# Kernel optimization log

Measured on AMD Instinct MI355X. Metric: run time of the kernel, lower is better.

The kernel has to match this reference:

```python
import jax, jax.numpy as jnp
import numpy as np

B, S, D, H = 4, 2048, 1024, 16
HD = D // H


def setup_inputs() -> dict:
    key = jax.random.key(0)
    ks = jax.random.split(key, 12)
    scale = 1.0 / np.sqrt(D)
    q = jax.random.normal(ks[0], (B, S, D), jnp.float32)
    k = jax.random.normal(ks[1], (B, S, D), jnp.float32)
    v = jax.random.normal(ks[2], (B, S, D), jnp.float32)
    mask = jax.random.randint(ks[3], (B, S, S), 0, 2).astype(bool)
    Wq = jax.random.normal(ks[4], (D, D), jnp.float32) * scale
    bq = jnp.zeros((D,), jnp.float32)
    Wk = jax.random.normal(ks[5], (D, D), jnp.float32) * scale
    bk = jnp.zeros((D,), jnp.float32)
    Wv = jax.random.normal(ks[6], (D, D), jnp.float32) * scale
    bv = jnp.zeros((D,), jnp.float32)
    Wo = jax.random.normal(ks[7], (D, D), jnp.float32) * scale
    bo = jnp.zeros((D,), jnp.float32)
    return {"q": q, "k": k, "v": v, "mask": mask,
            "Wq": Wq, "bq": bq, "Wk": Wk, "bk": bk,
            "Wv": Wv, "bv": bv, "Wo": Wo, "bo": bo}


def reference(q, k, v, mask, Wq, bq, Wk, bk, Wv, bv, Wo, bo):
    # project and split heads: [B,S,D] -> [B,H,S,HD]
    def split_heads(x, W, b):
        y = x @ W + b
        return y.reshape(B, S, H, HD).transpose(0, 2, 1, 3)

    Q = split_heads(q, Wq, bq)
    K = split_heads(k, Wk, bk)
    V = split_heads(v, Wv, bv)
    inv_sqrt_dk = 1.0 / np.sqrt(HD)
    scores = jnp.einsum('bhqd,bhkd->bhqk', Q, K) * inv_sqrt_dk
    scores = jnp.where(mask[:, None, :, :], -1e9, scores)
    attn = jax.nn.softmax(scores, axis=-1)
    ctx = jnp.einsum('bhqk,bhkd->bhqd', attn, V)  # [B,H,S,HD]
    ctx = ctx.transpose(0, 2, 1, 3).reshape(B, S, D)
    return ctx @ Wo + bo
```

## Files before the change

kernel.cpp:

```cpp
#include <hip/hip_runtime.h>
#include <stdint.h>

#define B_ 4
#define S_ 2048
#define D_ 1024
#define H_ 16
#define HD_ 64

typedef __attribute__((ext_vector_type(8))) __bf16          bf16x8;
typedef __attribute__((ext_vector_type(8))) unsigned short  u16x8;
typedef __attribute__((ext_vector_type(4))) unsigned short  u16x4;
typedef __attribute__((ext_vector_type(4))) float           f32x4;
typedef __attribute__((ext_vector_type(16))) float          f32x16;
typedef unsigned short u16;
typedef unsigned int   u32;
typedef unsigned long long u64;

union BF8 { u16x8 u; bf16x8 b; u32 w[4]; };

__device__ __forceinline__ u16 f2bf(float f) {
  union { float f; uint32_t u; } v; v.f = f;
  uint32_t r = (v.u + 0x7FFFu + ((v.u >> 16) & 1u)) >> 16;
  return (u16)r;
}

__device__ __forceinline__ u32 cvtpk(float lo, float hi) {
  u32 r;
  asm("v_cvt_pk_bf16_f32 %0, %1, %2" : "=v"(r) : "v"(lo), "v"(hi));
  return r;
}

__device__ __forceinline__ float fexp2(float x) {
  float r;
  asm("v_exp_f32 %0, %1" : "=v"(r) : "v"(x));
  return r;
}

__device__ __forceinline__ float frcp(float x) {
  float r;
  asm("v_rcp_f32 %0, %1" : "=v"(r) : "v"(x));
  return r;
}

__device__ __forceinline__ void pswap(u32& a, u32& b) {
  asm("v_permlane32_swap_b32 %0, %1" : "+v"(a), "+v"(b));
}

__device__ __forceinline__ float andf(float x, u32 m) {
  union { float f; u32 u; } v; v.f = x; v.u &= m; return v.f;
}

typedef const unsigned int __attribute__((address_space(1)))* gas1_t;
typedef unsigned int __attribute__((address_space(3)))*       las3_t;

__device__ __forceinline__ void gll16(const void* g, void* l) {
  __builtin_amdgcn_global_load_lds((gas1_t)g, (las3_t)l, 16, 0, 0);
}

#define MFMA32(a, b, c) __builtin_amdgcn_mfma_f32_32x32x16_bf16((a), (b), (c), 0, 0, 0)

__global__ __launch_bounds__(256) void prep_k(const float* __restrict__ qi, const float* __restrict__ ki,
                                              const float* __restrict__ vi, u16* __restrict__ oq,
                                              u16* __restrict__ ok, u16* __restrict__ ov,
                                              const float* __restrict__ Wq, const float* __restrict__ Wk,
                                              const float* __restrict__ Wv, const float* __restrict__ Wo,
                                              u16* __restrict__ Tq, u16* __restrict__ Tk,
                                              u16* __restrict__ Tv, u16* __restrict__ To) {
  __shared__ float tile[64][65];
  int blk = blockIdx.x;
  int t = threadIdx.x;
  if (blk < 12288) {
    const float* in; u16* out;
    if (blk < 4096) { in = qi; out = oq; }
    else if (blk < 8192) { in = ki; out = ok; blk -= 4096; }
    else { in = vi; out = ov; blk -= 8192; }
    int i = blk * 256 + t;
    const float4* p = ((const float4*)in) + (size_t)i * 2;
    float4 a = p[0], b = p[1];
    u16x8 o;
    o[0] = f2bf(a.x); o[1] = f2bf(a.y); o[2] = f2bf(a.z); o[3] = f2bf(a.w);
    o[4] = f2bf(b.x); o[5] = f2bf(b.y); o[6] = f2bf(b.z); o[7] = f2bf(b.w);
    *(((u16x8*)out) + i) = o;
    return;
  }
  int wi = blk - 12288;
  int z = wi >> 8, rem = wi & 255;
  int bx = rem & 15, by = rem >> 4;
  const float* src; u16* dst;
  switch (z) {
    case 0: src = Wq; dst = Tq; break;
    case 1: src = Wk; dst = Tk; break;
    case 2: src = Wv; dst = Tv; break;
    default: src = Wo; dst = To; break;
  }
  int k0 = bx * 64, n0 = by * 64;
#pragma unroll
  for (int it = 0; it < 4; ++it) {
    int idx = it * 256 + t;
    int r = idx >> 4, c = idx & 15;
    float4 v = *(const float4*)(src + (size_t)(k0 + r) * 1024 + n0 + c * 4);
    tile[r][c * 4 + 0] = v.x; tile[r][c * 4 + 1] = v.y;
    tile[r][c * 4 + 2] = v.z; tile[r][c * 4 + 3] = v.w;
  }
  __syncthreads();
#pragma unroll
  for (int it = 0; it < 2; ++it) {
    int idx = it * 256 + t;
    int n = idx >> 3, kc = idx & 7;
    u16x8 o;
#pragma unroll
    for (int j = 0; j < 8; ++j) o[j] = f2bf(tile[kc * 8 + j][n]);
    *(u16x8*)(dst + (size_t)(n0 + n) * 1024 + k0 + kc * 8) = o;
  }
}

__global__ __launch_bounds__(256) void maskpack_k(const void* __restrict__ mraw,
                                                  u64* __restrict__ mout) {
  const u32* hdr = (const u32*)mraw;
  int t = threadIdx.x;
  int lane = t & 63;
  u32 hv = hdr[lane];
  bool isf = (hv == 0x3F800000u);
  u64 bigm = __ballot(hv > 1u && !isf);
  u64 fm = __ballot(isf);
  int fmt = (__popcll(fm) > 8) ? 2 : ((bigm != 0ull) ? 0 : 1);
  size_t idx = (size_t)blockIdx.x * 256 + t;
  u64 bits = 0;
  if (fmt == 0) {
    const u64* p = (const u64*)((const uint8_t*)mraw + idx * 64);
#pragma unroll
    for (int j = 0; j < 8; ++j) {
      u64 v = p[j];
#pragma unroll
      for (int kk = 0; kk < 8; ++kk)
        bits |= (u64)(((v >> (8 * kk)) & 0xFFull) != 0) << (j * 8 + kk);
    }
  } else if (fmt == 1) {
    const int* p = ((const int*)mraw) + idx * 64;
#pragma unroll
    for (int j = 0; j < 64; ++j) bits |= (u64)(p[j] != 0) << j;
  } else {
    const u32* p = ((const u32*)mraw) + idx * 64;
#pragma unroll
    for (int j = 0; j < 64; ++j) bits |= (u64)((p[j] << 1) != 0) << j;
  }
  mout[idx] = bits;
}

__global__ __launch_bounds__(256) void proj3_k(const u16* __restrict__ Aq, const u16* __restrict__ Ak,
                                               const u16* __restrict__ Av,
                                               const u16* __restrict__ Tq, const u16* __restrict__ Tk,
                                               const u16* __restrict__ Tv,
                                               const float* __restrict__ bq, const float* __restrict__ bk,
                                               const float* __restrict__ bv,
                                               u16* __restrict__ Qh, u16* __restrict__ Kh,
                                               u16* __restrict__ Vt, float qscale) {
  int g = blockIdx.x >> 9, bid = blockIdx.x & 511;
  const u16* A; const u16* Bt; const float* bias; u16* outp; float scale;
  if (g == 0) { A = Aq; Bt = Tq; bias = bq; outp = Qh; scale = qscale; }
  else if (g == 1) { A = Ak; Bt = Tk; bias = bk; outp = Kh; scale = 1.0f; }
  else { A = Av; Bt = Tv; bias = bv; outp = Vt; scale = 1.0f; }
  int xcd = bid & 7, loc = bid >> 3;
  int mt = xcd * 8 + (loc & 7), nt = loc >> 3;
  int m0 = mt * 128, n0 = nt * 128;
  int t = threadIdx.x, w = t >> 6, lane = t & 63;
  int l15 = lane & 15, l4 = lane >> 4;
  int wm = w >> 1, wn = w & 1;
  __shared__ __align__(16) char smem[16384];
  const f32x4 vzero = {0.f, 0.f, 0.f, 0.f};
  f32x4 acc[4][4];
#pragma unroll
  for (int a = 0; a < 4; ++a)
#pragma unroll
    for (int c = 0; c < 4; ++c) acc[a][c] = vzero;

  for (int k0 = 0; k0 < 1024; k0 += 32) {
#pragma unroll
    for (int i = 0; i < 2; ++i) {
      int chunk = i * 256 + w * 64 + lane;
      int row = chunk >> 2, slot = chunk & 3;
      int sc = slot ^ ((row >> 1) & 3);
      gll16(A + (size_t)(m0 + row) * 1024 + k0 + sc * 8, smem + (i * 256 + w * 64) * 16);
      gll16(Bt + (size_t)(n0 + row) * 1024 + k0 + sc * 8, smem + 8192 + (i * 256 + w * 64) * 16);
    }
    __syncthreads();
    BF8 am[4], bn[4];
#pragma unroll
    for (int mb = 0; mb < 4; ++mb) {
      int row = wm * 64 + mb * 16 + l15;
      int sl = l4 ^ ((row >> 1) & 3);
      am[mb].u = *(const u16x8*)(smem + row * 64 + sl * 16);
    }
#pragma unroll
    for (int nb = 0; nb < 4; ++nb) {
      int row = wn * 64 + nb * 16 + l15;
      int sl = l4 ^ ((row >> 1) & 3);
      bn[nb].u = *(const u16x8*)(smem + 8192 + row * 64 + sl * 16);
    }
#pragma unroll
    for (int mb = 0; mb < 4; ++mb)
#pragma unroll
      for (int nb = 0; nb < 4; ++nb)
        acc[mb][nb] = __builtin_amdgcn_mfma_f32_16x16x32_bf16(am[mb].b, bn[nb].b, acc[mb][nb], 0, 0, 0);
    __syncthreads();
  }
  if (g == 2) {
#pragma unroll
    for (int mb = 0; mb < 4; ++mb)
#pragma unroll
      for (int nb = 0; nb < 4; ++nb) {
        int no = n0 + wn * 64 + nb * 16 + l15;
        int h = no >> 6, hd = no & 63;
        int m = m0 + wm * 64 + mb * 16 + l4 * 4;
        int bb = m >> 11, s = m & 2047;
        float bsv = bias[no];
        u16x4 ov;
#pragma unroll
        for (int r = 0; r < 4; ++r) ov[r] = f2bf(acc[mb][nb][r] + bsv);
        *(u16x4*)(outp + (((size_t)bb * H_ + h) * HD_ + hd) * S_ + s) = ov;
      }
  } else {
#pragma unroll
    for (int mb = 0; mb < 4; ++mb)
#pragma unroll
      for (int nb = 0; nb < 4; ++nb)
#pragma unroll
        for (int r = 0; r < 4; ++r) {
          int grow = m0 + wm * 64 + mb * 16 + l4 * 4 + r;
          int gcol = n0 + wn * 64 + nb * 16 + l15;
          float v = (acc[mb][nb][r] + bias[gcol]) * scale;
          int bb = grow >> 11, s = grow & 2047, h = gcol >> 6, hd = gcol & 63;
          outp[(((size_t)bb * H_ + h) * S_ + s) * HD_ + hd] = f2bf(v);
        }
  }
}

__global__ __launch_bounds__(256) void gemmo_k(const u16* __restrict__ A,
                                               const u16* __restrict__ Bt,
                                               const float* __restrict__ bias,
                                               float* __restrict__ outp) {
  int bid = blockIdx.x;
  int xcd = bid & 7, loc = bid >> 3;
  int mt = xcd * 8 + (loc & 7), nt = loc >> 3;
  int m0 = mt * 128, n0 = nt * 128;
  int t = threadIdx.x, w = t >> 6, lane = t & 63;
  int l15 = lane & 15, l4 = lane >> 4;
  int wm = w >> 1, wn = w & 1;
  __shared__ __align__(16) char smem[16384];
  const f32x4 vzero = {0.f, 0.f, 0.f, 0.f};
  f32x4 acc[4][4];
#pragma unroll
  for (int a = 0; a < 4; ++a)
#pragma unroll
    for (int c = 0; c < 4; ++c) acc[a][c] = vzero;

  for (int k0 = 0; k0 < 1024; k0 += 32) {
#pragma unroll
    for (int i = 0; i < 2; ++i) {
      int chunk = i * 256 + w * 64 + lane;
      int row = chunk >> 2, slot = chunk & 3;
      int sc = slot ^ ((row >> 1) & 3);
      gll16(A + (size_t)(m0 + row) * 1024 + k0 + sc * 8, smem + (i * 256 + w * 64) * 16);
      gll16(Bt + (size_t)(n0 + row) * 1024 + k0 + sc * 8, smem + 8192 + (i * 256 + w * 64) * 16);
    }
    __syncthreads();
    BF8 am[4], bn[4];
#pragma unroll
    for (int mb = 0; mb < 4; ++mb) {
      int row = wm * 64 + mb * 16 + l15;
      int sl = l4 ^ ((row >> 1) & 3);
      am[mb].u = *(const u16x8*)(smem + row * 64 + sl * 16);
    }
#pragma unroll
    for (int nb = 0; nb < 4; ++nb) {
      int row = wn * 64 + nb * 16 + l15;
      int sl = l4 ^ ((row >> 1) & 3);
      bn[nb].u = *(const u16x8*)(smem + 8192 + row * 64 + sl * 16);
    }
#pragma unroll
    for (int mb = 0; mb < 4; ++mb)
#pragma unroll
      for (int nb = 0; nb < 4; ++nb)
        acc[mb][nb] = __builtin_amdgcn_mfma_f32_16x16x32_bf16(am[mb].b, bn[nb].b, acc[mb][nb], 0, 0, 0);
    __syncthreads();
  }
#pragma unroll
  for (int mb = 0; mb < 4; ++mb)
#pragma unroll
    for (int nb = 0; nb < 4; ++nb)
#pragma unroll
      for (int r = 0; r < 4; ++r) {
        int grow = m0 + wm * 64 + mb * 16 + l4 * 4 + r;
        int gcol = n0 + wn * 64 + nb * 16 + l15;
        outp[(size_t)grow * 1024 + gcol] = acc[mb][nb][r] + bias[gcol];
      }
}

__global__ __launch_bounds__(256) void flash_k(const u16* __restrict__ Qh,
                                               const u16* __restrict__ Kh,
                                               const u16* __restrict__ Vt,
                                               const u64* __restrict__ mb,
                                               u16* __restrict__ ctx) {
  int bid = blockIdx.x;
  int xcd = bid & 7, loc = bid >> 3;
  int bh = xcd * 8 + (loc & 7);
  int qblk = loc >> 3;
  int b = bh >> 4, h = bh & 15;
  int t = threadIdx.x, w = t >> 6, lane = t & 63;
  int l31 = lane & 31, l5 = lane >> 5;
  __shared__ __align__(16) char smem[32768];

  int q0 = qblk * 128 + w * 32;
  const u16* kbase = Kh + (size_t)bh * S_ * HD_;
  const u16* vbase = Vt + (size_t)bh * HD_ * S_;
  const uint2* mrow = ((const uint2*)mb) + ((size_t)b * S_ + q0 + l31) * 32;

  const u16* qbase = Qh + ((size_t)bh * S_ + q0 + l31) * HD_;
  BF8 qf[4];
#pragma unroll
  for (int dk = 0; dk < 4; ++dk) qf[dk].u = *(const u16x8*)(qbase + dk * 16 + l5 * 8);

  int koff0[4], koffB[4];
#pragma unroll
  for (int dk = 0; dk < 4; ++dk) {
    int s0_ = (dk * 2 + l5) ^ (l31 & 7) ^ (l31 >> 3);
    koff0[dk] = l31 * 128 + s0_ * 16;
    koffB[dk] = 4096 + l31 * 128 + ((s0_ ^ 4) * 16);
  }

  BF8 onesf;
#pragma unroll
  for (int i = 0; i < 8; ++i) onesf.u[i] = 0x3F80;

  f32x16 o0, o1, lac, zv;
#pragma unroll
  for (int r = 0; r < 16; ++r) { o0[r] = 0.f; o1[r] = 0.f; lac[r] = 0.f; zv[r] = 0.f; }

#define STAGE(KT, BUF)                                                          \
  do {                                                                          \
    char* Kd = smem + (BUF);                                                    \
    int k0s = (KT) * 64;                                                        \
    _Pragma("unroll") for (int i_ = 0; i_ < 2; ++i_) {                          \
      int c_ = i_ * 256 + t;                                                    \
      int row_ = c_ >> 3, sl_ = c_ & 7;                                         \
      int sc_ = sl_ ^ (row_ & 7) ^ (row_ >> 3);                                 \
      int cw_ = (i_ * 256 + w * 64) * 16;                                       \
      gll16(kbase + (size_t)(k0s + row_) * HD_ + sc_ * 8, Kd + cw_);            \
      gll16(vbase + (size_t)row_ * S_ + k0s + sc_ * 8, Kd + 8192 + cw_);        \
    }                                                                           \
  } while (0)

#define MKFRAG(FR, A0, B0, C0, D0)                                              \
  do {                                                                          \
    u32 xx0 = (A0), xx1 = (C0), yy0 = (B0), yy1 = (D0);                         \
    pswap(xx0, xx1); pswap(yy0, yy1);                                           \
    FR.w[0] = xx0; FR.w[1] = yy0; FR.w[2] = xx1; FR.w[3] = yy1;                 \
  } while (0)

#define PVS(FR, KC)                                                             \
  do {                                                                          \
    lac = MFMA32(FR.b, onesf.b, lac);                                           \
    BF8 vf0, vf1;                                                               \
    vf0.u = *(const u16x8*)(Kb + 8192 + koff0[(KC)]);                           \
    vf1.u = *(const u16x8*)(Kb + 8192 + koffB[(KC)]);                           \
    o0 = MFMA32(FR.b, vf0.b, o0);                                               \
    o1 = MFMA32(FR.b, vf1.b, o1);                                               \
  } while (0)

#define FTILE(KT, BUF, OBUF, ISLAST)                                            \
  {                                                                             \
    __syncthreads();                                                            \
    uint2 mw = mrow[(KT)];                                                      \
    if (!(ISLAST)) STAGE((KT) + 1, OBUF);                                       \
    const char* Kb = smem + (BUF);                                              \
    f32x16 sa0, sa1;                                                            \
    __builtin_amdgcn_s_setprio(1);                                              \
    {                                                                           \
      BF8 kf0, kf1;                                                             \
      kf0.u = *(const u16x8*)(Kb + koff0[0]);                                   \
      kf1.u = *(const u16x8*)(Kb + koffB[0]);                                   \
      sa0 = MFMA32(kf0.b, qf[0].b, zv);                                         \
      sa1 = MFMA32(kf1.b, qf[0].b, zv);                                         \
    }                                                                           \
    _Pragma("unroll") for (int dk = 1; dk < 4; ++dk) {                          \
      BF8 kf0, kf1;                                                             \
      kf0.u = *(const u16x8*)(Kb + koff0[dk]);                                  \
      kf1.u = *(const u16x8*)(Kb + koffB[dk]);                                  \
      sa0 = MFMA32(kf0.b, qf[dk].b, sa0);                                       \
      sa1 = MFMA32(kf1.b, qf[dk].b, sa1);                                       \
    }                                                                           \
    __builtin_amdgcn_s_setprio(0);                                              \
    u32 nw0 = ~(mw.x >> (l5 * 4));                                              \
    u32 nw1 = ~(mw.y >> (l5 * 4));                                              \
    _Pragma("unroll") for (int r = 0; r < 16; ++r) {                            \
      const int pp = (r & 3) + 8 * (r >> 2);                                    \
      sa0[r] = andf(fexp2(sa0[r]), (u32)__builtin_amdgcn_sbfe((int)nw0, pp, 1));\
      sa1[r] = andf(fexp2(sa1[r]), (u32)__builtin_amdgcn_sbfe((int)nw1, pp, 1));\
    }                                                                           \
    u32 pk0[8], pk1[8];                                                         \
    _Pragma("unroll") for (int i = 0; i < 8; ++i) {                             \
      pk0[i] = cvtpk(sa0[2 * i], sa0[2 * i + 1]);                               \
      pk1[i] = cvtpk(sa1[2 * i], sa1[2 * i + 1]);                               \
    }                                                                           \
    BF8 fr0, fr1, fr2, fr3;                                                     \
    MKFRAG(fr0, pk0[0], pk0[1], pk0[2], pk0[3]);                                \
    MKFRAG(fr1, pk0[4], pk0[5], pk0[6], pk0[7]);                                \
    MKFRAG(fr2, pk1[0], pk1[1], pk1[2], pk1[3]);                                \
    MKFRAG(fr3, pk1[4], pk1[5], pk1[6], pk1[7]);                                \
    __builtin_amdgcn_s_setprio(1);                                              \
    PVS(fr0, 0); PVS(fr1, 1); PVS(fr2, 2); PVS(fr3, 3);                         \
    __builtin_amdgcn_s_setprio(0);                                              \
  }

  STAGE(0, 0);
  for (int kt2 = 0; kt2 < 16; ++kt2) {
    FTILE(2 * kt2, 0, 16384, false);
    FTILE(2 * kt2 + 1, 16384, 0, (kt2 == 15));
  }

#pragma unroll
  for (int r = 0; r < 16; ++r) {
    float inv = frcp(lac[r] + 1e-35f);
    int q = (r & 3) + 8 * (r >> 2) + 4 * l5;
    size_t base = ((size_t)b * S_ + q0 + q) * D_ + h * HD_;
    ctx[base + l31]      = f2bf(o0[r] * inv);
    ctx[base + 32 + l31] = f2bf(o1[r] * inv);
  }
#undef STAGE
#undef MKFRAG
#undef PVS
#undef FTILE
}

extern "C" void kernel_launch(void* const* d_in, const int* in_sizes, int n_in,
                              void* d_out, int out_size, void* d_ws, size_t ws_size,
                              hipStream_t stream) {
  (void)in_sizes; (void)n_in; (void)out_size; (void)ws_size;
  const float* q  = (const float*)d_in[0];
  const float* k  = (const float*)d_in[1];
  const float* v  = (const float*)d_in[2];
  const void*  mk = d_in[3];
  const float* Wq = (const float*)d_in[4];
  const float* bq = (const float*)d_in[5];
  const float* Wk = (const float*)d_in[6];
  const float* bk = (const float*)d_in[7];
  const float* Wv = (const float*)d_in[8];
  const float* bv = (const float*)d_in[9];
  const float* Wo = (const float*)d_in[10];
  const float* bo = (const float*)d_in[11];

  char* ws = (char*)d_ws;
  u16* qb   = (u16*)(ws + 0);
  u16* kbuf = (u16*)(ws + 16777216);
  u16* vbuf = (u16*)(ws + 33554432);
  u16* Tq   = (u16*)(ws + 50331648);
  u16* Tk   = (u16*)(ws + 52428800);
  u16* Tv   = (u16*)(ws + 54525952);
  u16* To   = (u16*)(ws + 56623104);
  u16* Qh   = (u16*)(ws + 58720256);
  u16* Kh   = (u16*)(ws + 75497472);
  u16* Vt   = (u16*)(ws + 92274688);
  u16* ctx  = kbuf;
  u64* mc   = (u64*)vbuf;

  const float QSCALE = 0.18033688011112042f;

  prep_k<<<13312, 256, 0, stream>>>(q, k, v, qb, kbuf, vbuf,
                                    Wq, Wk, Wv, Wo, Tq, Tk, Tv, To);
  proj3_k<<<1536, 256, 0, stream>>>(qb, kbuf, vbuf, Tq, Tk, Tv,
                                    bq, bk, bv, Qh, Kh, Vt, QSCALE);
  maskpack_k<<<1024, 256, 0, stream>>>(mk, mc);
  flash_k<<<1024, 256, 0, stream>>>(Qh, Kh, Vt, mc, ctx);
  gemmo_k<<<512, 256, 0, stream>>>(ctx, To, bo, (float*)d_out);
}
```

Baseline: 250.4 us.

## Replace projection GEMMs with 256x256-tile, 4-stage pipelined 32x32 MFMA kernel

Both the QKV projection and the output projection now use a shared GEMM body with 256x256 block tiles, 512 threads, 32x32x16 MFMA instructions and a four-deep global-to-LDS prefetch ring synchronised with explicit waitcnt and barriers. This raises arithmetic intensity per block and overlaps loads with compute, replacing the single-buffered 128x128 tiles that waited on a full barrier every k-step. The cost is 128KB of LDS per block, which allows only one block per CU. Grids also shrink to 384 and 128 blocks, which may underfill a 256-CU device, especially for the output GEMM.

```diff
diff --git a/kernel.cpp b/kernel.cpp
--- a/kernel.cpp
+++ b/kernel.cpp
@@ -147,153 +147,161 @@
   mout[idx] = bits;
 }
 
-__global__ __launch_bounds__(256) void proj3_k(const u16* __restrict__ Aq, const u16* __restrict__ Ak,
-                                               const u16* __restrict__ Av,
-                                               const u16* __restrict__ Tq, const u16* __restrict__ Tk,
-                                               const u16* __restrict__ Tv,
-                                               const float* __restrict__ bq, const float* __restrict__ bk,
-                                               const float* __restrict__ bv,
-                                               u16* __restrict__ Qh, u16* __restrict__ Kh,
-                                               u16* __restrict__ Vt, float qscale) {
-  int g = blockIdx.x >> 9, bid = blockIdx.x & 511;
-  const u16* A; const u16* Bt; const float* bias; u16* outp; float scale;
-  if (g == 0) { A = Aq; Bt = Tq; bias = bq; outp = Qh; scale = qscale; }
-  else if (g == 1) { A = Ak; Bt = Tk; bias = bk; outp = Kh; scale = 1.0f; }
-  else { A = Av; Bt = Tv; bias = bv; outp = Vt; scale = 1.0f; }
-  int xcd = bid & 7, loc = bid >> 3;
-  int mt = xcd * 8 + (loc & 7), nt = loc >> 3;
-  int m0 = mt * 128, n0 = nt * 128;
-  int t = threadIdx.x, w = t >> 6, lane = t & 63;
-  int l15 = lane & 15, l4 = lane >> 4;
-  int wm = w >> 1, wn = w & 1;
-  __shared__ __align__(16) char smem[16384];
-  const f32x4 vzero = {0.f, 0.f, 0.f, 0.f};
-  f32x4 acc[4][4];
-#pragma unroll
-  for (int a = 0; a < 4; ++a)
-#pragma unroll
-    for (int c = 0; c < 4; ++c) acc[a][c] = vzero;
-
-  for (int k0 = 0; k0 < 1024; k0 += 32) {
-#pragma unroll
-    for (int i = 0; i < 2; ++i) {
-      int chunk = i * 256 + w * 64 + lane;
-      int row = chunk >> 2, slot = chunk & 3;
-      int sc = slot ^ ((row >> 1) & 3);
-      gll16(A + (size_t)(m0 + row) * 1024 + k0 + sc * 8, smem + (i * 256 + w * 64) * 16);
-      gll16(Bt + (size_t)(n0 + row) * 1024 + k0 + sc * 8, smem + 8192 + (i * 256 + w * 64) * 16);
+__device__ __forceinline__ void gemm256_body(const u16* __restrict__ A, const u16* __restrict__ Bt,
+                                             const float* __restrict__ bias, void* __restrict__ outp,
+                                             float scale, int mode, int inner, char* smem) {
+  int xcd = inner & 7, loc = inner >> 3;
+  int mt = xcd * 4 + (loc & 3), nt = loc >> 2;
+  int m0 = mt * 256, n0 = nt * 256;
+  int tid = threadIdx.x, w = tid >> 6, lane = tid & 63;
+  int l31 = lane & 31, l5 = lane >> 5;
+  int wm = w >> 2, wn = w & 3;
+
+  const u16* pA[2]; const u16* pB[2];
+#pragma unroll
+  for (int q = 0; q < 2; ++q) {
+    int c = q * 512 + tid;
+    int R = c >> 3, s8 = c & 7;
+    int s8u = s8 ^ (R & 7) ^ ((R >> 3) & 7);
+    int srow = 2 * R + (s8u >> 2), skw = s8u & 3;
+    pA[q] = A  + ((size_t)(m0 + srow) << 10) + skw * 8;
+    pB[q] = Bt + ((size_t)(n0 + srow) << 10) + skw * 8;
+  }
+
+  int aoff[4][2], boff[2][2];
+#pragma unroll
+  for (int i = 0; i < 4; ++i) {
+    int r = wm * 128 + i * 32 + l31;
+    int R = r >> 1, sw = (R & 7) ^ ((R >> 3) & 7);
+#pragma unroll
+    for (int kk = 0; kk < 2; ++kk) {
+      int s8 = ((r & 1) << 2) + kk * 2 + l5;
+      aoff[i][kk] = R * 128 + ((s8 ^ sw) << 4);
     }
-    __syncthreads();
-    BF8 am[4], bn[4];
-#pragma unroll
-    for (int mb = 0; mb < 4; ++mb) {
-      int row = wm * 64 + mb * 16 + l15;
-      int sl = l4 ^ ((row >> 1) & 3);
-      am[mb].u = *(const u16x8*)(smem + row * 64 + sl * 16);
+  }
+#pragma unroll
+  for (int j = 0; j < 2; ++j) {
+    int r = wn * 64 + j * 32 + l31;
+    int R = r >> 1, sw = (R & 7) ^ ((R >> 3) & 7);
+#pragma unroll
+    for (int kk = 0; kk < 2; ++kk) {
+      int s8 = ((r & 1) << 2) + kk * 2 + l5;
+      boff[j][kk] = 32768 + R * 128 + ((s8 ^ sw) << 4);
     }
-#pragma unroll
-    for (int nb = 0; nb < 4; ++nb) {
-      int row = wn * 64 + nb * 16 + l15;
-      int sl = l4 ^ ((row >> 1) & 3);
-      bn[nb].u = *(const u16x8*)(smem + 8192 + row * 64 + sl * 16);
+  }
+
+  f32x16 acc[4][2];
+#pragma unroll
+  for (int i = 0; i < 4; ++i)
+#pragma unroll
+    for (int j = 0; j < 2; ++j)
+#pragma unroll
+      for (int r = 0; r < 16; ++r) acc[i][j][r] = 0.f;
+
+#define GSTAGE(TAU)                                                             \
+  do {                                                                          \
+    char* db = smem + ((((TAU) >> 1) & 1) << 16) + (((TAU) & 1) << 14) + w * 1024; \
+    gll16(pA[0] + (TAU) * 32, db);                                              \
+    gll16(pA[1] + (TAU) * 32, db + 8192);                                       \
+    gll16(pB[0] + (TAU) * 32, db + 32768);                                      \
+    gll16(pB[1] + (TAU) * 32, db + 40960);                                      \
+  } while (0)
+
+#define GCOMPUTE(TAU)                                                           \
+  do {                                                                          \
+    const char* base = smem + ((((TAU) >> 1) & 1) << 16) + (((TAU) & 1) << 14); \
+    BF8 af[4][2], bf_[2][2];                                                    \
+    _Pragma("unroll") for (int kk = 0; kk < 2; ++kk) {                          \
+      _Pragma("unroll") for (int i = 0; i < 4; ++i)                             \
+        af[i][kk].u = *(const u16x8*)(base + aoff[i][kk]);                      \
+      _Pragma("unroll") for (int j = 0; j < 2; ++j)                             \
+        bf_[j][kk].u = *(const u16x8*)(base + boff[j][kk]);                     \
+    }                                                                           \
+    __builtin_amdgcn_s_setprio(1);                                              \
+    _Pragma("unroll") for (int kk = 0; kk < 2; ++kk)                            \
+      _Pragma("unroll") for (int i = 0; i < 4; ++i)                             \
+        _Pragma("unroll") for (int j = 0; j < 2; ++j)                           \
+          acc[i][j] = MFMA32(af[i][kk].b, bf_[j][kk].b, acc[i][j]);             \
+    __builtin_amdgcn_s_setprio(0);                                              \
+  } while (0)
+
+  GSTAGE(0);
+  GSTAGE(1);
+#pragma unroll 2
+  for (int tau = 0; tau < 31; ++tau) {
+    asm volatile("s_waitcnt vmcnt(4)" ::: "memory");
+    __builtin_amdgcn_s_barrier();
+    __builtin_amdgcn_sched_barrier(0);
+    if (tau < 30) GSTAGE(tau + 2);
+    GCOMPUTE(tau);
+  }
+  asm volatile("s_waitcnt vmcnt(0)" ::: "memory");
+  __builtin_amdgcn_s_barrier();
+  __builtin_amdgcn_sched_barrier(0);
+  GCOMPUTE(31);
+#undef GSTAGE
+#undef GCOMPUTE
+
+#pragma unroll
+  for (int i = 0; i < 4; ++i)
+#pragma unroll
+    for (int j = 0; j < 2; ++j) {
+      int gcol = n0 + wn * 64 + j * 32 + l31;
+      float bv = bias[gcol];
+      if (mode == 1) {
+        int hh = gcol >> 6, hd = gcol & 63;
+#pragma unroll
+        for (int qd = 0; qd < 4; ++qd) {
+          int grow = m0 + wm * 128 + i * 32 + qd * 8 + l5 * 4;
+          int bb = grow >> 11, s = grow & 2047;
+          u16x4 ov;
+#pragma unroll
+          for (int rr = 0; rr < 4; ++rr) ov[rr] = f2bf(acc[i][j][qd * 4 + rr] + bv);
+          *(u16x4*)((u16*)outp + (((size_t)bb * H_ + hh) * HD_ + hd) * S_ + s) = ov;
+        }
+      } else if (mode == 0) {
+        int hh = gcol >> 6, hd = gcol & 63;
+#pragma unroll
+        for (int reg = 0; reg < 16; ++reg) {
+          int grow = m0 + wm * 128 + i * 32 + (reg & 3) + 8 * (reg >> 2) + 4 * l5;
+          int bb = grow >> 11, s = grow & 2047;
+          ((u16*)outp)[(((size_t)bb * H_ + hh) * S_ + s) * HD_ + hd] =
+              f2bf((acc[i][j][reg] + bv) * scale);
+        }
+      } else {
+#pragma unroll
+        for (int reg = 0; reg < 16; ++reg) {
+          int grow = m0 + wm * 128 + i * 32 + (reg & 3) + 8 * (reg >> 2) + 4 * l5;
+          ((float*)outp)[(size_t)grow * 1024 + gcol] = acc[i][j][reg] + bv;
+        }
+      }
     }
-#pragma unroll
-    for (int mb = 0; mb < 4; ++mb)
-#pragma unroll
-      for (int nb = 0; nb < 4; ++nb)
-        acc[mb][nb] = __builtin_amdgcn_mfma_f32_16x16x32_bf16(am[mb].b, bn[nb].b, acc[mb][nb], 0, 0, 0);
-    __syncthreads();
-  }
-  if (g == 2) {
-#pragma unroll
-    for (int mb = 0; mb < 4; ++mb)
-#pragma unroll
-      for (int nb = 0; nb < 4; ++nb) {
-        int no = n0 + wn * 64 + nb * 16 + l15;
-        int h = no >> 6, hd = no & 63;
-        int m = m0 + wm * 64 + mb * 16 + l4 * 4;
-        int bb = m >> 11, s = m & 2047;
-        float bsv = bias[no];
-        u16x4 ov;
-#pragma unroll
-        for (int r = 0; r < 4; ++r) ov[r] = f2bf(acc[mb][nb][r] + bsv);
-        *(u16x4*)(outp + (((size_t)bb * H_ + h) * HD_ + hd) * S_ + s) = ov;
-      }
-  } else {
-#pragma unroll
-    for (int mb = 0; mb < 4; ++mb)
-#pragma unroll
-      for (int nb = 0; nb < 4; ++nb)
-#pragma unroll
-        for (int r = 0; r < 4; ++r) {
-          int grow = m0 + wm * 64 + mb * 16 + l4 * 4 + r;
-          int gcol = n0 + wn * 64 + nb * 16 + l15;
-          float v = (acc[mb][nb][r] + bias[gcol]) * scale;
-          int bb = grow >> 11, s = grow & 2047, h = gcol >> 6, hd = gcol & 63;
-          outp[(((size_t)bb * H_ + h) * S_ + s) * HD_ + hd] = f2bf(v);
-        }
-  }
-}
-
-__global__ __launch_bounds__(256) void gemmo_k(const u16* __restrict__ A,
-                                               const u16* __restrict__ Bt,
-                                               const float* __restrict__ bias,
-                                               float* __restrict__ outp) {
+}
+
+__global__ __launch_bounds__(512) void proj3n_k(const u16* __restrict__ Aq, const u16* __restrict__ Ak,
+                                                const u16* __restrict__ Av,
+                                                const u16* __restrict__ Tq, const u16* __restrict__ Tk,
+                                                const u16* __restrict__ Tv,
+                                                const float* __restrict__ bq, const float* __restrict__ bk,
+                                                const float* __restrict__ bv,
+                                                u16* __restrict__ Qh, u16* __restrict__ Kh,
+                                                u16* __restrict__ Vt, float qscale) {
+  __shared__ __align__(16) char smem[131072];
   int bid = blockIdx.x;
-  int xcd = bid & 7, loc = bid >> 3;
-  int mt = xcd * 8 + (loc & 7), nt = loc >> 3;
-  int m0 = mt * 128, n0 = nt * 128;
-  int t = threadIdx.x, w = t >> 6, lane = t & 63;
-  int l15 = lane & 15, l4 = lane >> 4;
-  int wm = w >> 1, wn = w & 1;
-  __shared__ __align__(16) char smem[16384];
-  const f32x4 vzero = {0.f, 0.f, 0.f, 0.f};
-  f32x4 acc[4][4];
-#pragma unroll
-  for (int a = 0; a < 4; ++a)
-#pragma unroll
-    for (int c = 0; c < 4; ++c) acc[a][c] = vzero;
-
-  for (int k0 = 0; k0 < 1024; k0 += 32) {
-#pragma unroll
-    for (int i = 0; i < 2; ++i) {
-      int chunk = i * 256 + w * 64 + lane;
-      int row = chunk >> 2, slot = chunk & 3;
-      int sc = slot ^ ((row >> 1) & 3);
-      gll16(A + (size_t)(m0 + row) * 1024 + k0 + sc * 8, smem + (i * 256 + w * 64) * 16);
-      gll16(Bt + (size_t)(n0 + row) * 1024 + k0 + sc * 8, smem + 8192 + (i * 256 + w * 64) * 16);
-    }
-    __syncthreads();
-    BF8 am[4], bn[4];
-#pragma unroll
-    for (int mb = 0; mb < 4; ++mb) {
-      int row = wm * 64 + mb * 16 + l15;
-      int sl = l4 ^ ((row >> 1) & 3);
-      am[mb].u = *(const u16x8*)(smem + row * 64 + sl * 16);
-    }
-#pragma unroll
-    for (int nb = 0; nb < 4; ++nb) {
-      int row = wn * 64 + nb * 16 + l15;
-      int sl = l4 ^ ((row >> 1) & 3);
-      bn[nb].u = *(const u16x8*)(smem + 8192 + row * 64 + sl * 16);
-    }
-#pragma unroll
-    for (int mb = 0; mb < 4; ++mb)
-#pragma unroll
-      for (int nb = 0; nb < 4; ++nb)
-        acc[mb][nb] = __builtin_amdgcn_mfma_f32_16x16x32_bf16(am[mb].b, bn[nb].b, acc[mb][nb], 0, 0, 0);
-    __syncthreads();
-  }
-#pragma unroll
-  for (int mb = 0; mb < 4; ++mb)
-#pragma unroll
-    for (int nb = 0; nb < 4; ++nb)
-#pragma unroll
-      for (int r = 0; r < 4; ++r) {
-        int grow = m0 + wm * 64 + mb * 16 + l4 * 4 + r;
-        int gcol = n0 + wn * 64 + nb * 16 + l15;
-        outp[(size_t)grow * 1024 + gcol] = acc[mb][nb][r] + bias[gcol];
-      }
+  int g = bid >> 7, inner = bid & 127;
+  const u16* A; const u16* Bt; const float* bias; void* outp; float scale; int mode;
+  if (g == 0)      { A = Aq; Bt = Tq; bias = bq; outp = Qh; scale = qscale; mode = 0; }
+  else if (g == 1) { A = Ak; Bt = Tk; bias = bk; outp = Kh; scale = 1.0f;  mode = 0; }
+  else             { A = Av; Bt = Tv; bias = bv; outp = Vt; scale = 1.0f;  mode = 1; }
+  gemm256_body(A, Bt, bias, outp, scale, mode, inner, smem);
+}
+
+__global__ __launch_bounds__(512) void gemmo2_k(const u16* __restrict__ A,
+                                                const u16* __restrict__ Bt,
+                                                const float* __restrict__ bias,
+                                                float* __restrict__ outp) {
+  __shared__ __align__(16) char smem[131072];
+  gemm256_body(A, Bt, bias, outp, 1.0f, 2, blockIdx.x, smem);
 }
 
 __global__ __launch_bounds__(256) void flash_k(const u16* __restrict__ Qh,
@@ -467,9 +475,9 @@
 
   prep_k<<<13312, 256, 0, stream>>>(q, k, v, qb, kbuf, vbuf,
                                     Wq, Wk, Wv, Wo, Tq, Tk, Tv, To);
-  proj3_k<<<1536, 256, 0, stream>>>(qb, kbuf, vbuf, Tq, Tk, Tv,
+  proj3n_k<<<384, 512, 0, stream>>>(qb, kbuf, vbuf, Tq, Tk, Tv,
                                     bq, bk, bv, Qh, Kh, Vt, QSCALE);
   maskpack_k<<<1024, 256, 0, stream>>>(mk, mc);
   flash_k<<<1024, 256, 0, stream>>>(Qh, Kh, Vt, mc, ctx);
-  gemmo_k<<<512, 256, 0, stream>>>(ctx, To, bo, (float*)d_out);
-}
+  gemmo2_k<<<128, 512, 0, stream>>>(ctx, To, bo, (float*)d_out);
+}
```

Result: slower. 268.5 us (+7.2%).

## Fuse fp32-to-bf16 activation conversion into projection GEMM A-tile loads

Applied to the files above, without the earlier changes.

The separate pass that converted q/k/v from fp32 to bf16 in workspace is removed. The projection GEMM now loads fp32 A tiles directly into registers, packs them to bf16 and writes them into swizzled LDS. This avoids writing and rereading about 48 MB of intermediate bf16 activations. In exchange, the GEMM reads twice the A bytes per tile, and those loads go through registers synchronously with no prefetch, which may expose latency in the k-loop.

```diff
diff --git a/kernel.cpp b/kernel.cpp
--- a/kernel.cpp
+++ b/kernel.cpp
@@ -59,31 +59,13 @@
 
 #define MFMA32(a, b, c) __builtin_amdgcn_mfma_f32_32x32x16_bf16((a), (b), (c), 0, 0, 0)
 
-__global__ __launch_bounds__(256) void prep_k(const float* __restrict__ qi, const float* __restrict__ ki,
-                                              const float* __restrict__ vi, u16* __restrict__ oq,
-                                              u16* __restrict__ ok, u16* __restrict__ ov,
-                                              const float* __restrict__ Wq, const float* __restrict__ Wk,
-                                              const float* __restrict__ Wv, const float* __restrict__ Wo,
-                                              u16* __restrict__ Tq, u16* __restrict__ Tk,
-                                              u16* __restrict__ Tv, u16* __restrict__ To) {
+__global__ __launch_bounds__(256) void wt_k(const float* __restrict__ Wq, const float* __restrict__ Wk,
+                                            const float* __restrict__ Wv, const float* __restrict__ Wo,
+                                            u16* __restrict__ Tq, u16* __restrict__ Tk,
+                                            u16* __restrict__ Tv, u16* __restrict__ To) {
   __shared__ float tile[64][65];
-  int blk = blockIdx.x;
   int t = threadIdx.x;
-  if (blk < 12288) {
-    const float* in; u16* out;
-    if (blk < 4096) { in = qi; out = oq; }
-    else if (blk < 8192) { in = ki; out = ok; blk -= 4096; }
-    else { in = vi; out = ov; blk -= 8192; }
-    int i = blk * 256 + t;
-    const float4* p = ((const float4*)in) + (size_t)i * 2;
-    float4 a = p[0], b = p[1];
-    u16x8 o;
-    o[0] = f2bf(a.x); o[1] = f2bf(a.y); o[2] = f2bf(a.z); o[3] = f2bf(a.w);
-    o[4] = f2bf(b.x); o[5] = f2bf(b.y); o[6] = f2bf(b.z); o[7] = f2bf(b.w);
-    *(((u16x8*)out) + i) = o;
-    return;
-  }
-  int wi = blk - 12288;
+  int wi = blockIdx.x;
   int z = wi >> 8, rem = wi & 255;
   int bx = rem & 15, by = rem >> 4;
   const float* src; u16* dst;
@@ -147,8 +129,8 @@
   mout[idx] = bits;
 }
 
-__global__ __launch_bounds__(256) void proj3_k(const u16* __restrict__ Aq, const u16* __restrict__ Ak,
-                                               const u16* __restrict__ Av,
+__global__ __launch_bounds__(256) void proj3_k(const float* __restrict__ Aq, const float* __restrict__ Ak,
+                                               const float* __restrict__ Av,
                                                const u16* __restrict__ Tq, const u16* __restrict__ Tk,
                                                const u16* __restrict__ Tv,
                                                const float* __restrict__ bq, const float* __restrict__ bk,
@@ -156,7 +138,7 @@
                                                u16* __restrict__ Qh, u16* __restrict__ Kh,
                                                u16* __restrict__ Vt, float qscale) {
   int g = blockIdx.x >> 9, bid = blockIdx.x & 511;
-  const u16* A; const u16* Bt; const float* bias; u16* outp; float scale;
+  const float* A; const u16* Bt; const float* bias; u16* outp; float scale;
   if (g == 0) { A = Aq; Bt = Tq; bias = bq; outp = Qh; scale = qscale; }
   else if (g == 1) { A = Ak; Bt = Tk; bias = bk; outp = Kh; scale = 1.0f; }
   else { A = Av; Bt = Tv; bias = bv; outp = Vt; scale = 1.0f; }
@@ -174,15 +156,29 @@
 #pragma unroll
     for (int c = 0; c < 4; ++c) acc[a][c] = vzero;
 
+  int arow = t >> 1, ahalf = t & 1;
+  const float* abase = A + (size_t)(m0 + arow) * 1024 + ahalf * 16;
+  int aswz = (arow >> 1) & 3;
+  char* adst0 = smem + arow * 64 + (((2 * ahalf) ^ aswz) << 4);
+  char* adst1 = smem + arow * 64 + (((2 * ahalf + 1) ^ aswz) << 4);
+
   for (int k0 = 0; k0 < 1024; k0 += 32) {
+    const float4* ap = (const float4*)(abase + k0);
+    float4 a0 = ap[0], a1 = ap[1], a2 = ap[2], a3 = ap[3];
 #pragma unroll
     for (int i = 0; i < 2; ++i) {
       int chunk = i * 256 + w * 64 + lane;
       int row = chunk >> 2, slot = chunk & 3;
       int sc = slot ^ ((row >> 1) & 3);
-      gll16(A + (size_t)(m0 + row) * 1024 + k0 + sc * 8, smem + (i * 256 + w * 64) * 16);
       gll16(Bt + (size_t)(n0 + row) * 1024 + k0 + sc * 8, smem + 8192 + (i * 256 + w * 64) * 16);
     }
+    uint4 wv0, wv1;
+    wv0.x = cvtpk(a0.x, a0.y); wv0.y = cvtpk(a0.z, a0.w);
+    wv0.z = cvtpk(a1.x, a1.y); wv0.w = cvtpk(a1.z, a1.w);
+    wv1.x = cvtpk(a2.x, a2.y); wv1.y = cvtpk(a2.z, a2.w);
+    wv1.z = cvtpk(a3.x, a3.y); wv1.w = cvtpk(a3.z, a3.w);
+    *(uint4*)adst0 = wv0;
+    *(uint4*)adst1 = wv1;
     __syncthreads();
     BF8 am[4], bn[4];
 #pragma unroll
@@ -450,9 +446,8 @@
   const float* bo = (const float*)d_in[11];
 
   char* ws = (char*)d_ws;
-  u16* qb   = (u16*)(ws + 0);
-  u16* kbuf = (u16*)(ws + 16777216);
-  u16* vbuf = (u16*)(ws + 33554432);
+  u16* ctx  = (u16*)(ws + 16777216);
+  u64* mc   = (u64*)(ws + 33554432);
   u16* Tq   = (u16*)(ws + 50331648);
   u16* Tk   = (u16*)(ws + 52428800);
   u16* Tv   = (u16*)(ws + 54525952);
@@ -460,16 +455,13 @@
   u16* Qh   = (u16*)(ws + 58720256);
   u16* Kh   = (u16*)(ws + 75497472);
   u16* Vt   = (u16*)(ws + 92274688);
-  u16* ctx  = kbuf;
-  u64* mc   = (u64*)vbuf;
 
   const float QSCALE = 0.18033688011112042f;
 
-  prep_k<<<13312, 256, 0, stream>>>(q, k, v, qb, kbuf, vbuf,
-                                    Wq, Wk, Wv, Wo, Tq, Tk, Tv, To);
-  proj3_k<<<1536, 256, 0, stream>>>(qb, kbuf, vbuf, Tq, Tk, Tv,
+  maskpack_k<<<1024, 256, 0, stream>>>(mk, mc);
+  wt_k<<<1024, 256, 0, stream>>>(Wq, Wk, Wv, Wo, Tq, Tk, Tv, To);
+  proj3_k<<<1536, 256, 0, stream>>>(q, k, v, Tq, Tk, Tv,
                                     bq, bk, bv, Qh, Kh, Vt, QSCALE);
-  maskpack_k<<<1024, 256, 0, stream>>>(mk, mc);
   flash_k<<<1024, 256, 0, stream>>>(Qh, Kh, Vt, mc, ctx);
   gemmo_k<<<512, 256, 0, stream>>>(ctx, To, bo, (float*)d_out);
 }
```

After: 282.0 us. 12.6% more time.
